# Optimization experiments

Measured on AMD Instinct MI355X. Metric: run time of the kernel, lower is better.

The kernel has to match this reference:

```python
import jax, jax.numpy as jnp
import numpy as np

B_GR = 128    # graphs per batch
N0 = 512      # nodes per graph before pooling
E_PER = 4096  # edges per graph (kept static; pooled-away edges get weight 0)
H = 128       # hidden
F = 128       # num_features (== hidden)
C = 10        # num_classes
K_HOP = 3     # Jacobi polynomial order (hop_num)
A_J, B_J = 1.0, 1.0
EPS = 1e-5


def _bn(h, g, b):
    # training-mode BatchNorm1d: batch stats, biased variance
    m = jnp.mean(h, 0)
    v = jnp.mean((h - m) ** 2, 0)
    return (h - m) * jax.lax.rsqrt(v + EPS) * g + b


def _forward(x, convW, convb, bnW, bnB, bn7W, bn7B, attW, theta,
             lin1W, lin1b, lin2W, lin2b, lin3W, lin3b, src, dst):
    w = jnp.ones((src.shape[0],), x.dtype)  # edge weights; 0 => filtered edge
    n = N0
    h = x
    reads = []
    for i in range(5):
        N = B_GR * n
        # symmetric GCN normalization with self loops on the weighted graph
        deg = jax.ops.segment_sum(w, dst, num_segments=N) + 1.0
        dinv = jax.lax.rsqrt(deg)
        enorm = dinv[src] * dinv[dst] * w   # per-edge norm [E]
        snorm = dinv * dinv                 # self-loop norm [N]
        prop = lambda m_: jax.ops.segment_sum(enorm[:, None] * m_[src], dst, num_segments=N) + m_ * snorm[:, None]
        pvec = lambda v_: jax.ops.segment_sum(enorm * v_[src], dst, num_segments=N) + v_ * snorm
        # GCNConv -> BN -> ReLU
        h = prop(h @ convW[i]) + convb[i]
        h = jax.nn.relu(_bn(h, bnW[i], bnB[i]))
        # JacobiPool: Jacobi-polynomial diffusion of attention scores
        s0 = h @ attW[i]                    # [N]
        polys = [s0, 0.5 * ((A_J - B_J) * s0 + (A_J + B_J + 2.0) * pvec(s0))]
        for kk in range(2, K_HOP + 1):
            c0 = 2 * kk * (kk + A_J + B_J) * (2 * kk + A_J + B_J - 2)
            c1 = (2 * kk + A_J + B_J - 1) * (2 * kk + A_J + B_J) * (2 * kk + A_J + B_J - 2)
            c2 = (2 * kk + A_J + B_J - 1) * (A_J * A_J - B_J * B_J)
            c3 = 2 * (kk + A_J - 1) * (kk + B_J - 1) * (2 * kk + A_J + B_J)
            polys.append((c1 * pvec(polys[-1]) + c2 * polys[-1] - c3 * polys[-2]) / c0)
        score = sum(theta[i, j] * polys[j] for j in range(K_HOP + 1))
        # top-k node selection per graph (ratio 0.5 -> static k)
        k = n // 2
        _, idx = jax.lax.top_k(score.reshape(B_GR, n), k)
        sel = (idx + (jnp.arange(B_GR) * n)[:, None]).reshape(-1)  # global node ids [B*k]
        h = h[sel] * jnp.tanh(score[sel])[:, None]
        # remap/filter edges to surviving nodes (masked, static edge count)
        new_id = jnp.full((N,), -1, jnp.int32).at[sel].set(jnp.arange(B_GR * k, dtype=jnp.int32))
        ns, nd = new_id[src], new_id[dst]
        valid = (ns >= 0) & (nd >= 0) & (w > 0)
        w = valid.astype(x.dtype)
        src = jnp.where(valid, ns, 0)
        dst = jnp.where(valid, nd, 0)
        # readout: global max pool || global mean pool per graph
        xg = h.reshape(B_GR, k, H)
        reads.append(jnp.concatenate([xg.max(1), xg.mean(1)], -1))
        n = k
    g = sum(reads) / 5.0                    # [B, 2H]
    g = jax.nn.relu(_bn(g @ lin1W + lin1b, bnW[5], bnB[5]))
    g = jax.nn.relu(_bn(g @ lin2W + lin2b, bn7W, bn7B))
    return jax.nn.log_softmax(g @ lin3W + lin3b, -1)


def setup_inputs() -> dict:
    key = jax.random.key(0)
    ks = jax.random.split(key, 8)
    N = B_GR * N0
    E = B_GR * E_PER
    rng = np.random.default_rng(0)
    off = np.repeat(np.arange(B_GR, dtype=np.int32) * N0, E_PER)
    src = jnp.asarray(off + rng.integers(0, N0, E).astype(np.int32))
    dst = jnp.asarray(off + rng.integers(0, N0, E).astype(np.int32))
    s = 1.0 / np.sqrt(H)
    return {
        "x": jax.random.normal(ks[0], (N, F), jnp.float32),
        "convW": jax.random.normal(ks[1], (5, H, H), jnp.float32) * s,
        "convb": jnp.zeros((5, H), jnp.float32),
        "bnW": jnp.ones((6, H), jnp.float32),
        "bnB": jnp.zeros((6, H), jnp.float32),
        "bn7W": jnp.ones((H // 2,), jnp.float32),
        "bn7B": jnp.zeros((H // 2,), jnp.float32),
        "attW": jax.random.normal(ks[2], (5, H), jnp.float32) * s,
        "theta": jax.random.normal(ks[3], (5, K_HOP + 1), jnp.float32) * 0.5,
        "lin1W": jax.random.normal(ks[4], (2 * H, H), jnp.float32) * (1.0 / np.sqrt(2 * H)),
        "lin1b": jnp.zeros((H,), jnp.float32),
        "lin2W": jax.random.normal(ks[5], (H, H // 2), jnp.float32) * s,
        "lin2b": jnp.zeros((H // 2,), jnp.float32),
        "lin3W": jax.random.normal(ks[6], (H // 2, C), jnp.float32) * (1.0 / np.sqrt(H // 2)),
        "lin3b": jnp.zeros((C,), jnp.float32),
        "src": src,
        "dst": dst,
    }


def reference(x, convW, convb, bnW, bnB, bn7W, bn7B, attW, theta,
              lin1W, lin1b, lin2W, lin2b, lin3W, lin3b, src, dst):
    return _forward(x, convW, convb, bnW, bnB, bn7W, bn7B, attW, theta,
                    lin1W, lin1b, lin2W, lin2b, lin3W, lin3b, src, dst)
```

## Files before the change

kernel.cpp:

```cpp
#include <hip/hip_runtime.h>
#include <hip/hip_bf16.h>

#define B_GRAPH 128
#define ETOT    (128*4096)
#define N0G     (128*512)
#define HF      128

__global__ __launch_bounds__(256) void k_init(const int* __restrict__ s_in, const int* __restrict__ d_in_,
                                              int* __restrict__ srcw, int* __restrict__ dstw,
                                              float* __restrict__ wv, int2* __restrict__ csr,
                                              int2* __restrict__ rb2, float* __restrict__ dinvv,
                                              float* __restrict__ gacc, float* __restrict__ statsH,
                                              float* __restrict__ stats0, float* __restrict__ stats1){
    int g = blockIdx.x, t = threadIdx.x;
    __shared__ int cnt[512];
    __shared__ int cur[512];
    __shared__ float dvl[512];
    for (int l = t; l < 512; l += 256) cnt[l] = 0;
    gacc[g*256 + t] = 0.f;
    if (g == 0){
        statsH[t] = 0.f; if (t < 128) statsH[256+t] = 0.f;
        stats0[t] = 0.f; stats1[t] = 0.f;
    }
    __syncthreads();
    for (int j = t; j < 4096; j += 256){
        int e = g*4096 + j;
        int sg = s_in[e], dg = d_in_[e];
        srcw[e] = sg; dstw[e] = dg; wv[e] = 1.f;
        atomicAdd(&cnt[dg & 511], 1);
    }
    __syncthreads();
    int c0 = cnt[2*t], c1 = cnt[2*t+1];
    int pairsum = c0 + c1;
    cur[t] = pairsum;
    __syncthreads();
    for (int off = 1; off < 256; off <<= 1){
        int a = (t >= off) ? cur[t-off] : 0;
        __syncthreads();
        cur[t] += a;
        __syncthreads();
    }
    int begpair = cur[t] - pairsum;
    __syncthreads();
    cur[2*t]   = begpair;
    cur[2*t+1] = begpair + c0;
    __syncthreads();
    for (int l = t; l < 512; l += 256){
        rb2[g*512 + l] = make_int2(g*4096 + cur[l], cnt[l]);
        float dv = rsqrtf((float)cnt[l] + 1.f);
        dvl[l] = dv;
        dinvv[g*512 + l] = dv;
    }
    __syncthreads();
    for (int j = t; j < 4096; j += 256){
        int e = g*4096 + j;
        int sg = srcw[e], dl = dstw[e] & 511;
        int p = atomicAdd(&cur[dl], 1);
        csr[g*4096 + p] = make_int2(sg, __float_as_int(dvl[sg & 511]));
    }
}

__global__ __launch_bounds__(256) void k_gemm(const float* __restrict__ A, const float* __restrict__ Wg,
                                              float* __restrict__ C){
    __shared__ float Ws[64*HF];
    int tx = threadIdx.x & 15, ty = threadIdx.x >> 4;
    int r0 = blockIdx.x*64 + ty*4, c0 = tx*4;
    float acc[4][8];
    #pragma unroll
    for (int j=0;j<4;++j)
        #pragma unroll
        for (int l=0;l<8;++l) acc[j][l] = 0.f;
    for (int kh = 0; kh < 2; ++kh){
        __syncthreads();
        {
            float4* d4 = (float4*)Ws;
            const float4* s4 = (const float4*)(Wg + kh*64*HF);
            for (int i = threadIdx.x; i < 64*HF/4; i += 256) d4[i] = s4[i];
        }
        __syncthreads();
        for (int k4 = 0; k4 < 16; ++k4){
            float4 av[4];
            #pragma unroll
            for (int j=0;j<4;++j)
                av[j] = *(const float4*)(A + (size_t)(r0+j)*HF + kh*64 + k4*4);
            #pragma unroll
            for (int kk=0; kk<4; ++kk){
                int kl = k4*4 + kk;
                float4 w0 = *(const float4*)(Ws + kl*HF + c0);
                float4 w1 = *(const float4*)(Ws + kl*HF + c0 + 64);
                #pragma unroll
                for (int j=0;j<4;++j){
                    float a = reinterpret_cast<const float*>(&av[j])[kk];
                    acc[j][0] += a*w0.x; acc[j][1] += a*w0.y; acc[j][2] += a*w0.z; acc[j][3] += a*w0.w;
                    acc[j][4] += a*w1.x; acc[j][5] += a*w1.y; acc[j][6] += a*w1.z; acc[j][7] += a*w1.w;
                }
            }
        }
    }
    #pragma unroll
    for (int j=0;j<4;++j){
        *(float4*)(C + (size_t)(r0+j)*HF + c0)      = make_float4(acc[j][0],acc[j][1],acc[j][2],acc[j][3]);
        *(float4*)(C + (size_t)(r0+j)*HF + c0 + 64) = make_float4(acc[j][4],acc[j][5],acc[j][6],acc[j][7]);
    }
}

__global__ __launch_bounds__(256) void k_prop(const float* __restrict__ Y, const float* __restrict__ cb,
                                              const int2* __restrict__ rb2, const int2* __restrict__ cp,
                                              const float* __restrict__ dinv,
                                              float* __restrict__ X, int n, int lb, int Nn){
    int xcd = blockIdx.x & 7, c = blockIdx.x >> 3;
    int g = xcd*16 + (c >> lb);
    int m = c & ((1 << lb) - 1);
    int v = g*n + m*8 + (threadIdx.x >> 5);
    int f4 = threadIdx.x & 31;
    float dv = dinv[v];
    float4 y = *(const float4*)(Y + (size_t)v*HF + f4*4);
    float4 acc = make_float4(0.f, 0.f, 0.f, 0.f);
    int2 rb = rb2[v];
    int e0 = rb.x, e1 = rb.x + rb.y;
    for (int j = e0; j < e1; ++j){
        int2 e = cp[j];
        int s = e.x & (Nn - 1);
        float en = __int_as_float(e.y);
        float4 h = *(const float4*)(Y + (size_t)s*HF + f4*4);
        acc.x += en*h.x; acc.y += en*h.y; acc.z += en*h.z; acc.w += en*h.w;
    }
    int f = f4*4;
    acc.x = y.x*dv*dv + dv*acc.x + cb[f];
    acc.y = y.y*dv*dv + dv*acc.y + cb[f+1];
    acc.z = y.z*dv*dv + dv*acc.z + cb[f+2];
    acc.w = y.w*dv*dv + dv*acc.w + cb[f+3];
    *(float4*)(X + (size_t)v*HF + f) = acc;
}

__global__ __launch_bounds__(256) void k_bnstats(const float* __restrict__ X, float* __restrict__ stats){
    int c = threadIdx.x & 127, h = threadIdx.x >> 7;
    int r0 = blockIdx.x * 256;
    float s = 0.f, s2 = 0.f;
    for (int r = r0 + h; r < r0 + 256; r += 2){
        float x = X[(size_t)r*HF + c];
        s += x; s2 += x*x;
    }
    __shared__ float l1[256], l2[256];
    l1[threadIdx.x] = s; l2[threadIdx.x] = s2;
    __syncthreads();
    if (threadIdx.x < 128){
        atomicAdd(&stats[c],     l1[threadIdx.x] + l1[threadIdx.x+128]);
        atomicAdd(&stats[128+c], l2[threadIdx.x] + l2[threadIdx.x+128]);
    }
}

__global__ __launch_bounds__(1024, 4) void k_conv(
    const float* __restrict__ A, const float* __restrict__ Wg, const float* __restrict__ cb,
    const int2* __restrict__ rb2, const int2* __restrict__ cp, const float* __restrict__ dinv,
    float* __restrict__ G, float* __restrict__ X, float* __restrict__ stats,
    int n, int Nn)
{
    int g = blockIdx.x, t = threadIdx.x;
    __shared__ float Ws[64*HF];
    __shared__ float red[32*HF];
    int sub = t >> 8;
    int t8  = t & 255;
    int tx = t8 & 15, ty = t8 >> 4;
    int nT = (n + 255) >> 8;
    for (int tile = 0; tile < nT; ++tile){
        int r0 = tile*256 + sub*64 + ty*4;
        bool act = (r0 < n);
        float acc[4][8];
        #pragma unroll
        for (int j=0;j<4;++j)
            #pragma unroll
            for (int l=0;l<8;++l) acc[j][l] = 0.f;
        for (int kh = 0; kh < 2; ++kh){
            __syncthreads();
            {
                float4* d4 = (float4*)Ws;
                const float4* s4 = (const float4*)(Wg + kh*64*HF);
                #pragma unroll
                for (int i = 0; i < 2; ++i) d4[t + i*1024] = s4[t + i*1024];
            }
            __syncthreads();
            if (act){
                int c0 = tx*4;
                for (int k4 = 0; k4 < 16; ++k4){
                    float4 av[4];
                    #pragma unroll
                    for (int j=0;j<4;++j)
                        av[j] = *(const float4*)(A + ((size_t)g*n + r0 + j)*HF + kh*64 + k4*4);
                    #pragma unroll
                    for (int kk=0; kk<4; ++kk){
                        int kl = k4*4 + kk;
                        float4 w0 = *(const float4*)(Ws + kl*HF + c0);
                        float4 w1 = *(const float4*)(Ws + kl*HF + c0 + 64);
                        #pragma unroll
                        for (int j=0;j<4;++j){
                            float a = reinterpret_cast<const float*>(&av[j])[kk];
                            acc[j][0] += a*w0.x; acc[j][1] += a*w0.y; acc[j][2] += a*w0.z; acc[j][3] += a*w0.w;
                            acc[j][4] += a*w1.x; acc[j][5] += a*w1.y; acc[j][6] += a*w1.z; acc[j][7] += a*w1.w;
                        }
                    }
                }
            }
        }
        if (act){
            int c0 = tx*4;
            #pragma unroll
            for (int j=0;j<4;++j){
                *(float4*)(G + ((size_t)g*n + r0 + j)*HF + c0)      = make_float4(acc[j][0],acc[j][1],acc[j][2],acc[j][3]);
                *(float4*)(G + ((size_t)g*n + r0 + j)*HF + c0 + 64) = make_float4(acc[j][4],acc[j][5],acc[j][6],acc[j][7]);
            }
        }
    }
    __syncthreads();
    int f4 = t & 31;
    int f = f4*4;
    float4 s  = make_float4(0.f,0.f,0.f,0.f);
    float4 s2 = make_float4(0.f,0.f,0.f,0.f);
    float cb0 = cb[f], cb1 = cb[f+1], cb2 = cb[f+2], cb3 = cb[f+3];
    for (int l = t >> 5; l < n; l += 32){
        int v = g*n + l;
        float dv = dinv[v];
        float4 y = *(const float4*)(G + (size_t)v*HF + f);
        float4 acc = make_float4(0.f,0.f,0.f,0.f);
        int2 rb = rb2[v];
        int e0 = rb.x, e1 = rb.x + rb.y;
        for (int j = e0; j < e1; ++j){
            int2 e = cp[j];
            int sN = e.x & (Nn - 1);
            float en = __int_as_float(e.y);
            float4 h = *(const float4*)(G + (size_t)sN*HF + f);
            acc.x += en*h.x; acc.y += en*h.y; acc.z += en*h.z; acc.w += en*h.w;
        }
        acc.x = y.x*dv*dv + dv*acc.x + cb0;
        acc.y = y.y*dv*dv + dv*acc.y + cb1;
        acc.z = y.z*dv*dv + dv*acc.z + cb2;
        acc.w = y.w*dv*dv + dv*acc.w + cb3;
        *(float4*)(X + (size_t)v*HF + f) = acc;
        s.x += acc.x; s.y += acc.y; s.z += acc.z; s.w += acc.w;
        s2.x += acc.x*acc.x; s2.y += acc.y*acc.y; s2.z += acc.z*acc.z; s2.w += acc.w*acc.w;
    }
    int base = (t >> 5)*HF + f;
    __syncthreads();
    *(float4*)&red[base] = s;
    __syncthreads();
    if (t < 128){
        float a = 0.f;
        #pragma unroll
        for (int j = 0; j < 32; ++j) a += red[j*HF + t];
        atomicAdd(&stats[t], a);
    }
    __syncthreads();
    *(float4*)&red[base] = s2;
    __syncthreads();
    if (t < 128){
        float a = 0.f;
        #pragma unroll
        for (int j = 0; j < 32; ++j) a += red[j*HF + t];
        atomicAdd(&stats[128+t], a);
    }
}

__global__ __launch_bounds__(1024) void k_graph(
    const float* __restrict__ H, const float* __restrict__ stats,
    const float* __restrict__ gw, const float* __restrict__ gb,
    const float* __restrict__ aw, const float* __restrict__ th,
    const int2* __restrict__ rb2, int2* __restrict__ csr, const float* __restrict__ dinv,
    int* __restrict__ srcw, int* __restrict__ dstw, float* __restrict__ wv,
    float* __restrict__ P, float* __restrict__ gacc,
    int2* __restrict__ rb2n, float* __restrict__ dinvn, float* __restrict__ statsNext,
    float invN, float ca2, float cc2, float ca3, float cc3,
    int n, int last)
{
    int g = blockIdx.x, t = threadIdx.x;
    int k = n >> 1;
    __shared__ int2  eds[4096];
    __shared__ int2  rbl[512];
    __shared__ float dvv[512], p0[512], p1[512], p2[512];
    __shared__ float ss[512];
    __shared__ int   si[512];
    __shared__ float tss[256];
    __shared__ int   nid[512];
    __shared__ int   cntN[256], curN[256];
    __shared__ float dvn[256];
    __shared__ float bna[128], bnb[128];
    __shared__ float red[1024];

    if (t < 256) statsNext[t] = 0.f;
    if (t < 128){
        float mean = stats[t]*invN;
        float var  = stats[128+t]*invN - mean*mean;
        float iv   = rsqrtf(var + 1e-5f);
        bna[t] = iv*gw[t];
        bnb[t] = gb[t] - mean*iv*gw[t];
    }
    for (int l = t; l < n; l += 1024){
        int2 rb = rb2[g*n + l];
        rbl[l] = make_int2(rb.x - g*4096, rb.y);
        dvv[l] = dinv[g*n + l];
    }
    __syncthreads();
    int medg = rbl[n-1].x + rbl[n-1].y;
    for (int j = t; j < medg; j += 1024){
        int2 e = csr[g*4096 + j];
        eds[j] = make_int2(e.x & (n-1), e.y);
    }
    int lane = t & 63, wid = t >> 6;
    for (int l = wid; l < n; l += 16){
        const float* hp = H + ((size_t)g*n + l)*HF;
        float a0 = hp[lane], a1 = hp[lane+64];
        float v0 = fmaxf(a0*bna[lane]    + bnb[lane],    0.f) * aw[lane];
        float v1 = fmaxf(a1*bna[lane+64] + bnb[lane+64], 0.f) * aw[lane+64];
        float p = v0 + v1;
        for (int off = 32; off; off >>= 1) p += __shfl_down(p, off);
        if (lane == 0) p0[l] = p;
    }
    __syncthreads();
    for (int l = t; l < n; l += 1024){
        int2 rc = rbl[l];
        float acc = 0.f;
        for (int j = 0; j < rc.y; ++j){
            int2 e = eds[rc.x + j];
            acc += __int_as_float(e.y) * p0[e.x];
        }
        float dv = dvv[l];
        p1[l] = 2.f*(p0[l]*dv*dv + dv*acc);
    }
    __syncthreads();
    for (int l = t; l < n; l += 1024){
        int2 rc = rbl[l];
        float acc = 0.f;
        for (int j = 0; j < rc.y; ++j){
            int2 e = eds[rc.x + j];
            acc += __int_as_float(e.y) * p1[e.x];
        }
        float dv = dvv[l];
        p2[l] = ca2*(p1[l]*dv*dv + dv*acc) + cc2*p0[l];
    }
    __syncthreads();
    float t0v = th[0], t1v = th[1], t2c = th[2], t3v = th[3];
    for (int l = t; l < n; l += 1024){
        int2 rc = rbl[l];
        float acc = 0.f;
        for (int j = 0; j < rc.y; ++j){
            int2 e = eds[rc.x + j];
            acc += __int_as_float(e.y) * p2[e.x];
        }
        float dv = dvv[l];
        float tv = p2[l]*dv*dv + dv*acc;
        float p3 = ca3*tv + cc3*p1[l];
        ss[l] = t0v*p0[l] + t1v*p1[l] + t2c*p2[l] + t3v*p3;
        si[l] = l;
    }
    __syncthreads();
    for (int size = 2; size <= n; size <<= 1){
        for (int stride = size >> 1; stride > 0; stride >>= 1){
            for (int i = t; i < n; i += 1024){
                int j = i ^ stride;
                if (j > i){
                    bool asc = ((i & size) == 0);
                    float s1 = ss[i], s2 = ss[j];
                    int   i1 = si[i], i2 = si[j];
                    bool gt = (s1 < s2) || (s1 == s2 && i1 > i2);
                    if (gt == asc){ ss[i] = s2; ss[j] = s1; si[i] = i2; si[j] = i1; }
                }
            }
            __syncthreads();
        }
    }
    for (int l = t; l < n; l += 1024) nid[l] = -1;
    __syncthreads();
    for (int r = t; r < k; r += 1024){
        nid[si[r]] = r;
        tss[r] = tanhf(ss[r]);
    }
    __syncthreads();
    {
        int f = t & 127, rl = t >> 7;
        float af = bna[f], bf = bnb[f];
        float mx = -3.4e38f, sm = 0.f;
        for (int r = rl; r < k; r += 8){
            int old = si[r];
            float hv = H[((size_t)g*n + old)*HF + f];
            float v = fmaxf(hv*af + bf, 0.f) * tss[r];
            P[((size_t)g*k + r)*HF + f] = v;
            mx = fmaxf(mx, v); sm += v;
        }
        red[t] = mx;
        __syncthreads();
        if (t < 512) red[t] = fmaxf(red[t], red[t+512]);
        __syncthreads();
        if (t < 256) red[t] = fmaxf(red[t], red[t+256]);
        __syncthreads();
        if (t < 128) gacc[g*256 + t] += fmaxf(red[t], red[t+128]);
        __syncthreads();
        red[t] = sm;
        __syncthreads();
        if (t < 512) red[t] += red[t+512];
        __syncthreads();
        if (t < 256) red[t] += red[t+256];
        __syncthreads();
        if (t < 128) gacc[g*256 + 128 + t] += (red[t] + red[t+128]) / (float)k;
    }
    if (last) return;
    __syncthreads();
    if (t < k) cntN[t] = 0;
    __syncthreads();
    for (int j = t; j < 4096; j += 1024){
        int e = g*4096 + j;
        float we = wv[e];
        int valid = 0, ns = 0, nd = 0;
        if (we > 0.5f){
            int sl = srcw[e] & (n-1);
            int dl = dstw[e] & (n-1);
            ns = nid[sl]; nd = nid[dl];
            valid = (ns >= 0) && (nd >= 0);
        }
        if (valid){
            srcw[e] = g*k + ns; dstw[e] = g*k + nd; wv[e] = 1.f;
            atomicAdd(&cntN[nd], 1);
        } else {
            srcw[e] = 0; dstw[e] = 0; wv[e] = 0.f;
        }
    }
    __syncthreads();
    int c = (t < 256) ? ((t < k) ? cntN[t] : 0) : 0;
    if (t < 256) si[t] = c;
    __syncthreads();
    for (int off = 1; off < 256; off <<= 1){
        int a = 0;
        if (t < 256 && t >= off) a = si[t-off];
        __syncthreads();
        if (t < 256) si[t] += a;
        __syncthreads();
    }
    if (t < k){
        int beg = si[t] - c;
        rb2n[g*k + t] = make_int2(g*4096 + beg, c);
        float dv = rsqrtf((float)c + 1.f);
        dinvn[g*k + t] = dv;
        dvn[t] = dv;
        curN[t] = beg;
    }
    __syncthreads();
    for (int j = t; j < 4096; j += 1024){
        int e = g*4096 + j;
        if (wv[e] > 0.5f){
            int sg = srcw[e], dl = dstw[e] & (k-1);
            int p = atomicAdd(&curN[dl], 1);
            csr[g*4096 + p] = make_int2(sg, __float_as_int(dvn[sg & (k-1)]));
        }
    }
}

__global__ __launch_bounds__(256) void k_head1(const float* __restrict__ gacc, const float* __restrict__ W1,
                                               const float* __restrict__ b1, float* __restrict__ t1,
                                               float* __restrict__ sh){
    int r = blockIdx.x;
    int c = threadIdx.x & 127, h = threadIdx.x >> 7;
    __shared__ float gs[256];
    __shared__ float red[256];
    gs[threadIdx.x] = gacc[r*256 + threadIdx.x];
    __syncthreads();
    float s = 0.f;
    #pragma unroll
    for (int kk = 0; kk < 128; ++kk)
        s += gs[h*128 + kk] * W1[(h*128 + kk)*128 + c];
    red[threadIdx.x] = s;
    __syncthreads();
    if (h == 0){
        float v = (red[c] + red[c+128]) * 0.2f + b1[c];
        t1[r*128 + c] = v;
        atomicAdd(&sh[c], v);
        atomicAdd(&sh[128 + c], v*v);
    }
}
__global__ __launch_bounds__(128) void k_head2(const float* __restrict__ t1, const float* __restrict__ gw,
                                               const float* __restrict__ gb, const float* __restrict__ W2,
                                               const float* __restrict__ b2, float* __restrict__ sh,
                                               float* __restrict__ t2){
    int r = blockIdx.x, t = threadIdx.x;
    int cc = t & 63, h = t >> 6;
    __shared__ float row[128];
    __shared__ float red[128];
    {
        float mean = sh[t] * (1.f/128.f);
        float var  = sh[128+t]*(1.f/128.f) - mean*mean;
        float iv   = rsqrtf(var + 1e-5f);
        float v = (t1[r*128+t] - mean)*iv*gw[t] + gb[t];
        row[t] = fmaxf(v, 0.f);
    }
    __syncthreads();
    float s = 0.f;
    #pragma unroll
    for (int kk = 0; kk < 64; ++kk)
        s += row[h*64+kk] * W2[(h*64+kk)*64 + cc];
    red[t] = s;
    __syncthreads();
    if (h == 0){
        float v = red[cc] + red[cc+64] + b2[cc];
        t2[r*64+cc] = v;
        atomicAdd(&sh[256+cc], v);
        atomicAdd(&sh[320+cc], v*v);
    }
}
__global__ __launch_bounds__(64) void k_head3(const float* __restrict__ t2, const float* __restrict__ gw,
                                              const float* __restrict__ gb, const float* __restrict__ W3,
                                              const float* __restrict__ b3, const float* __restrict__ sh,
                                              float* __restrict__ out){
    int r = blockIdx.x, t = threadIdx.x;
    float mean = sh[256+t]*(1.f/128.f);
    float var  = sh[320+t]*(1.f/128.f) - mean*mean;
    float iv   = rsqrtf(var + 1e-5f);
    float v = fmaxf((t2[r*64+t]-mean)*iv*gw[t] + gb[t], 0.f);
    float lg[10];
    #pragma unroll
    for (int j = 0; j < 10; ++j){
        float p = v * W3[t*10 + j];
        for (int off = 32; off; off >>= 1) p += __shfl_down(p, off);
        lg[j] = p;
    }
    if (t == 0){
        float m = -3.4e38f;
        #pragma unroll
        for (int j = 0; j < 10; ++j){ lg[j] += b3[j]; m = fmaxf(m, lg[j]); }
        float se = 0.f;
        #pragma unroll
        for (int j = 0; j < 10; ++j) se += expf(lg[j] - m);
        float l = logf(se) + m;
        #pragma unroll
        for (int j = 0; j < 10; ++j) out[r*10 + j] = lg[j] - l;
    }
}

extern "C" void kernel_launch(void* const* d_in, const int* in_sizes, int n_in,
                              void* d_out, int out_size, void* d_ws, size_t ws_size,
                              hipStream_t stream){
    const float* x     = (const float*)d_in[0];
    const float* convW = (const float*)d_in[1];
    const float* convb = (const float*)d_in[2];
    const float* bnW   = (const float*)d_in[3];
    const float* bnB   = (const float*)d_in[4];
    const float* bn7W  = (const float*)d_in[5];
    const float* bn7B  = (const float*)d_in[6];
    const float* attW  = (const float*)d_in[7];
    const float* theta = (const float*)d_in[8];
    const float* lin1W = (const float*)d_in[9];
    const float* lin1b = (const float*)d_in[10];
    const float* lin2W = (const float*)d_in[11];
    const float* lin2b = (const float*)d_in[12];
    const float* lin3W = (const float*)d_in[13];
    const float* lin3b = (const float*)d_in[14];
    const int*   src0  = (const int*)d_in[15];
    const int*   dst0  = (const int*)d_in[16];

    char* base = (char*)d_ws;
    size_t off = 0;
    auto take = [&](size_t bytes) -> void* {
        void* p = base + off;
        off = (off + bytes + 255) & ~(size_t)255;
        return p;
    };
    float* bufGP = (float*)take((size_t)N0G*HF*4);
    float* bufH  = (float*)take((size_t)N0G*HF*4);
    int*   srcw  = (int*)  take((size_t)ETOT*4);
    int*   dstw  = (int*)  take((size_t)ETOT*4);
    float* w     = (float*)take((size_t)ETOT*4);
    int2*  csr_p = (int2*) take((size_t)ETOT*8);
    int2*  rb2A  = (int2*) take((size_t)N0G*8);
    int2*  rb2B  = (int2*) take((size_t)N0G*8);
    float* dinvA = (float*)take((size_t)N0G*4);
    float* dinvB = (float*)take((size_t)N0G*4);
    float* stats0= (float*)take(256*4);
    float* stats1= (float*)take(256*4);
    float* gacc  = (float*)take((size_t)B_GRAPH*256*4);
    float* t1    = (float*)take((size_t)B_GRAPH*128*4);
    float* t2    = (float*)take((size_t)B_GRAPH*64*4);
    float* statsH= (float*)take(384*4);

    auto coef = [](int kk, float& ca, float& cc){
        double a = 1.0, b = 1.0;
        double c0 = 2.0*kk*(kk+a+b)*(2.0*kk+a+b-2.0);
        double c1 = (2.0*kk+a+b-1.0)*(2.0*kk+a+b)*(2.0*kk+a+b-2.0);
        double c3 = 2.0*(kk+a-1.0)*(kk+b-1.0)*(2.0*kk+a+b);
        ca = (float)(c1/c0); cc = (float)(-c3/c0);
    };
    float ca2, cc2, ca3, cc3;
    coef(2, ca2, cc2);
    coef(3, ca3, cc3);

    k_init<<<B_GRAPH, 256, 0, stream>>>(src0, dst0, srcw, dstw, w, csr_p, rb2A, dinvA,
                                        gacc, statsH, stats0, stats1);

    for (int i = 0; i < 5; ++i){
        int n = 512 >> i;
        int Nn = B_GRAPH*n;
        int2*  rb_cur = (i & 1) ? rb2B : rb2A;
        int2*  rb_nxt = (i & 1) ? rb2A : rb2B;
        float* dv_cur = (i & 1) ? dinvB : dinvA;
        float* dv_nxt = (i & 1) ? dinvA : dinvB;
        float* st_cur = (i & 1) ? stats1 : stats0;
        float* st_nxt = (i & 1) ? stats0 : stats1;
        const float* convA = (i == 0) ? x : bufGP;
        float* G = (i == 0) ? bufGP : (bufGP + (size_t)4*1024*1024);

        if (i == 0){
            k_gemm<<<Nn/64, 256, 0, stream>>>(convA, convW, G);
            k_prop<<<Nn/8, 256, 0, stream>>>(G, convb, rb_cur, csr_p, dv_cur, bufH, n, 6, Nn);
            k_bnstats<<<Nn/256, 256, 0, stream>>>(bufH, st_cur);
        } else {
            k_conv<<<B_GRAPH, 1024, 0, stream>>>(convA, convW + (size_t)i*HF*HF, convb + i*HF,
                                                 rb_cur, csr_p, dv_cur, G, bufH, st_cur, n, Nn);
        }
        k_graph<<<B_GRAPH, 1024, 0, stream>>>(bufH, st_cur, bnW + i*HF, bnB + i*HF, attW + i*HF,
                                              theta + i*4, rb_cur, csr_p, dv_cur,
                                              srcw, dstw, w, bufGP, gacc, rb_nxt, dv_nxt, st_nxt,
                                              1.0f/(float)Nn, ca2, cc2, ca3, cc3, n, (i == 4) ? 1 : 0);
    }

    k_head1<<<B_GRAPH, 256, 0, stream>>>(gacc, lin1W, lin1b, t1, statsH);
    k_head2<<<B_GRAPH, 128, 0, stream>>>(t1, bnW + 5*HF, bnB + 5*HF, lin2W, lin2b, statsH, t2);
    k_head3<<<B_GRAPH, 64, 0, stream>>>(t2, bn7W, bn7B, lin3W, lin3b, statsH, (float*)d_out);
}
```

Before: 484.8 us.

## Fuse next-level GCN conv into pooling kernel, rotating three stats buffers

```diff
diff --git a/kernel.cpp b/kernel.cpp
--- a/kernel.cpp
+++ b/kernel.cpp
@@ -11,7 +11,8 @@
                                               float* __restrict__ wv, int2* __restrict__ csr,
                                               int2* __restrict__ rb2, float* __restrict__ dinvv,
                                               float* __restrict__ gacc, float* __restrict__ statsH,
-                                              float* __restrict__ stats0, float* __restrict__ stats1){
+                                              float* __restrict__ st0, float* __restrict__ st1,
+                                              float* __restrict__ st2){
     int g = blockIdx.x, t = threadIdx.x;
     __shared__ int cnt[512];
     __shared__ int cur[512];
@@ -20,7 +21,7 @@
     gacc[g*256 + t] = 0.f;
     if (g == 0){
         statsH[t] = 0.f; if (t < 128) statsH[256+t] = 0.f;
-        stats0[t] = 0.f; stats1[t] = 0.f;
+        st0[t] = 0.f; st1[t] = 0.f; st2[t] = 0.f;
     }
     __syncthreads();
     for (int j = t; j < 4096; j += 256){
@@ -150,115 +151,16 @@
     }
 }
 
-__global__ __launch_bounds__(1024, 4) void k_conv(
-    const float* __restrict__ A, const float* __restrict__ Wg, const float* __restrict__ cb,
-    const int2* __restrict__ rb2, const int2* __restrict__ cp, const float* __restrict__ dinv,
-    float* __restrict__ G, float* __restrict__ X, float* __restrict__ stats,
-    int n, int Nn)
-{
-    int g = blockIdx.x, t = threadIdx.x;
-    __shared__ float Ws[64*HF];
-    __shared__ float red[32*HF];
-    int sub = t >> 8;
-    int t8  = t & 255;
-    int tx = t8 & 15, ty = t8 >> 4;
-    int nT = (n + 255) >> 8;
-    for (int tile = 0; tile < nT; ++tile){
-        int r0 = tile*256 + sub*64 + ty*4;
-        bool act = (r0 < n);
-        float acc[4][8];
-        #pragma unroll
-        for (int j=0;j<4;++j)
-            #pragma unroll
-            for (int l=0;l<8;++l) acc[j][l] = 0.f;
-        for (int kh = 0; kh < 2; ++kh){
-            __syncthreads();
-            {
-                float4* d4 = (float4*)Ws;
-                const float4* s4 = (const float4*)(Wg + kh*64*HF);
-                #pragma unroll
-                for (int i = 0; i < 2; ++i) d4[t + i*1024] = s4[t + i*1024];
-            }
-            __syncthreads();
-            if (act){
-                int c0 = tx*4;
-                for (int k4 = 0; k4 < 16; ++k4){
-                    float4 av[4];
-                    #pragma unroll
-                    for (int j=0;j<4;++j)
-                        av[j] = *(const float4*)(A + ((size_t)g*n + r0 + j)*HF + kh*64 + k4*4);
-                    #pragma unroll
-                    for (int kk=0; kk<4; ++kk){
-                        int kl = k4*4 + kk;
-                        float4 w0 = *(const float4*)(Ws + kl*HF + c0);
-                        float4 w1 = *(const float4*)(Ws + kl*HF + c0 + 64);
-                        #pragma unroll
-                        for (int j=0;j<4;++j){
-                            float a = reinterpret_cast<const float*>(&av[j])[kk];
-                            acc[j][0] += a*w0.x; acc[j][1] += a*w0.y; acc[j][2] += a*w0.z; acc[j][3] += a*w0.w;
-                            acc[j][4] += a*w1.x; acc[j][5] += a*w1.y; acc[j][6] += a*w1.z; acc[j][7] += a*w1.w;
-                        }
-                    }
-                }
-            }
-        }
-        if (act){
-            int c0 = tx*4;
-            #pragma unroll
-            for (int j=0;j<4;++j){
-                *(float4*)(G + ((size_t)g*n + r0 + j)*HF + c0)      = make_float4(acc[j][0],acc[j][1],acc[j][2],acc[j][3]);
-                *(float4*)(G + ((size_t)g*n + r0 + j)*HF + c0 + 64) = make_float4(acc[j][4],acc[j][5],acc[j][6],acc[j][7]);
-            }
-        }
-    }
-    __syncthreads();
-    int f4 = t & 31;
-    int f = f4*4;
-    float4 s  = make_float4(0.f,0.f,0.f,0.f);
-    float4 s2 = make_float4(0.f,0.f,0.f,0.f);
-    float cb0 = cb[f], cb1 = cb[f+1], cb2 = cb[f+2], cb3 = cb[f+3];
-    for (int l = t >> 5; l < n; l += 32){
-        int v = g*n + l;
-        float dv = dinv[v];
-        float4 y = *(const float4*)(G + (size_t)v*HF + f);
-        float4 acc = make_float4(0.f,0.f,0.f,0.f);
-        int2 rb = rb2[v];
-        int e0 = rb.x, e1 = rb.x + rb.y;
-        for (int j = e0; j < e1; ++j){
-            int2 e = cp[j];
-            int sN = e.x & (Nn - 1);
-            float en = __int_as_float(e.y);
-            float4 h = *(const float4*)(G + (size_t)sN*HF + f);
-            acc.x += en*h.x; acc.y += en*h.y; acc.z += en*h.z; acc.w += en*h.w;
-        }
-        acc.x = y.x*dv*dv + dv*acc.x + cb0;
-        acc.y = y.y*dv*dv + dv*acc.y + cb1;
-        acc.z = y.z*dv*dv + dv*acc.z + cb2;
-        acc.w = y.w*dv*dv + dv*acc.w + cb3;
-        *(float4*)(X + (size_t)v*HF + f) = acc;
-        s.x += acc.x; s.y += acc.y; s.z += acc.z; s.w += acc.w;
-        s2.x += acc.x*acc.x; s2.y += acc.y*acc.y; s2.z += acc.z*acc.z; s2.w += acc.w*acc.w;
-    }
-    int base = (t >> 5)*HF + f;
-    __syncthreads();
-    *(float4*)&red[base] = s;
-    __syncthreads();
-    if (t < 128){
-        float a = 0.f;
-        #pragma unroll
-        for (int j = 0; j < 32; ++j) a += red[j*HF + t];
-        atomicAdd(&stats[t], a);
-    }
-    __syncthreads();
-    *(float4*)&red[base] = s2;
-    __syncthreads();
-    if (t < 128){
-        float a = 0.f;
-        #pragma unroll
-        for (int j = 0; j < 32; ++j) a += red[j*HF + t];
-        atomicAdd(&stats[128+t], a);
-    }
-}
+union KSmem {
+    struct {
+        int2  eds[4096]; int2 rbl[512];
+        float dvv[512], p0[512], p1[512], p2[512];
+        float ss[512]; int si[512]; float tss[256]; int nid[512];
+        int   cntN[256], curN[256]; float dvn[256];
+        float bna[128], bnb[128]; float red[1024];
+    } gr;
+    struct { float Ws[64*HF]; float red[32*HF]; } cv;
+};
 
 __global__ __launch_bounds__(1024) void k_graph(
     const float* __restrict__ H, const float* __restrict__ stats,
@@ -267,89 +169,82 @@
     const int2* __restrict__ rb2, int2* __restrict__ csr, const float* __restrict__ dinv,
     int* __restrict__ srcw, int* __restrict__ dstw, float* __restrict__ wv,
     float* __restrict__ P, float* __restrict__ gacc,
-    int2* __restrict__ rb2n, float* __restrict__ dinvn, float* __restrict__ statsNext,
+    int2* __restrict__ rb2n, float* __restrict__ dinvn,
+    float* __restrict__ stZero, float* __restrict__ stAcc,
+    const float* __restrict__ Wnext, const float* __restrict__ cbNext,
+    float* __restrict__ Gnext, float* __restrict__ Hnext,
     float invN, float ca2, float cc2, float ca3, float cc3,
     int n, int last)
 {
     int g = blockIdx.x, t = threadIdx.x;
     int k = n >> 1;
-    __shared__ int2  eds[4096];
-    __shared__ int2  rbl[512];
-    __shared__ float dvv[512], p0[512], p1[512], p2[512];
-    __shared__ float ss[512];
-    __shared__ int   si[512];
-    __shared__ float tss[256];
-    __shared__ int   nid[512];
-    __shared__ int   cntN[256], curN[256];
-    __shared__ float dvn[256];
-    __shared__ float bna[128], bnb[128];
-    __shared__ float red[1024];
-
-    if (t < 256) statsNext[t] = 0.f;
+    __shared__ KSmem sm;
+
+    if (t < 256) stZero[t] = 0.f;
     if (t < 128){
         float mean = stats[t]*invN;
         float var  = stats[128+t]*invN - mean*mean;
         float iv   = rsqrtf(var + 1e-5f);
-        bna[t] = iv*gw[t];
-        bnb[t] = gb[t] - mean*iv*gw[t];
+        sm.gr.bna[t] = iv*gw[t];
+        sm.gr.bnb[t] = gb[t] - mean*iv*gw[t];
     }
     for (int l = t; l < n; l += 1024){
         int2 rb = rb2[g*n + l];
-        rbl[l] = make_int2(rb.x - g*4096, rb.y);
-        dvv[l] = dinv[g*n + l];
-    }
-    __syncthreads();
-    int medg = rbl[n-1].x + rbl[n-1].y;
+        sm.gr.rbl[l] = make_int2(rb.x - g*4096, rb.y);
+        sm.gr.dvv[l] = dinv[g*n + l];
+    }
+    __syncthreads();
+    int medg = sm.gr.rbl[n-1].x + sm.gr.rbl[n-1].y;
     for (int j = t; j < medg; j += 1024){
         int2 e = csr[g*4096 + j];
-        eds[j] = make_int2(e.x & (n-1), e.y);
+        sm.gr.eds[j] = make_int2(e.x & (n-1), e.y);
     }
     int lane = t & 63, wid = t >> 6;
     for (int l = wid; l < n; l += 16){
         const float* hp = H + ((size_t)g*n + l)*HF;
         float a0 = hp[lane], a1 = hp[lane+64];
-        float v0 = fmaxf(a0*bna[lane]    + bnb[lane],    0.f) * aw[lane];
-        float v1 = fmaxf(a1*bna[lane+64] + bnb[lane+64], 0.f) * aw[lane+64];
+        float v0 = fmaxf(a0*sm.gr.bna[lane]    + sm.gr.bnb[lane],    0.f) * aw[lane];
+        float v1 = fmaxf(a1*sm.gr.bna[lane+64] + sm.gr.bnb[lane+64], 0.f) * aw[lane+64];
         float p = v0 + v1;
         for (int off = 32; off; off >>= 1) p += __shfl_down(p, off);
-        if (lane == 0) p0[l] = p;
+        if (lane == 0) sm.gr.p0[l] = p;
     }
     __syncthreads();
     for (int l = t; l < n; l += 1024){
-        int2 rc = rbl[l];
+        int2 rc = sm.gr.rbl[l];
         float acc = 0.f;
         for (int j = 0; j < rc.y; ++j){
-            int2 e = eds[rc.x + j];
-            acc += __int_as_float(e.y) * p0[e.x];
-        }
-        float dv = dvv[l];
-        p1[l] = 2.f*(p0[l]*dv*dv + dv*acc);
+            int2 e = sm.gr.eds[rc.x + j];
+            acc += __int_as_float(e.y) * sm.gr.p0[e.x];
+        }
+        float dv = sm.gr.dvv[l];
+        sm.gr.p1[l] = 2.f*(sm.gr.p0[l]*dv*dv + dv*acc);
     }
     __syncthreads();
     for (int l = t; l < n; l += 1024){
-        int2 rc = rbl[l];
+        int2 rc = sm.gr.rbl[l];
         float acc = 0.f;
         for (int j = 0; j < rc.y; ++j){
-            int2 e = eds[rc.x + j];
-            acc += __int_as_float(e.y) * p1[e.x];
-        }
-        float dv = dvv[l];
-        p2[l] = ca2*(p1[l]*dv*dv + dv*acc) + cc2*p0[l];
+            int2 e = sm.gr.eds[rc.x + j];
+            acc += __int_as_float(e.y) * sm.gr.p1[e.x];
+        }
+        float dv = sm.gr.dvv[l];
+        sm.gr.p2[l] = ca2*(sm.gr.p1[l]*dv*dv + dv*acc) + cc2*sm.gr.p0[l];
     }
     __syncthreads();
     float t0v = th[0], t1v = th[1], t2c = th[2], t3v = th[3];
     for (int l = t; l < n; l += 1024){
-        int2 rc = rbl[l];
+        int2 rc = sm.gr.rbl[l];
         float acc = 0.f;
         for (int j = 0; j < rc.y; ++j){
-            int2 e = eds[rc.x + j];
-            acc += __int_as_float(e.y) * p2[e.x];
-        }
-        float dv = dvv[l];
-        float tv = p2[l]*dv*dv + dv*acc;
-        float p3 = ca3*tv + cc3*p1[l];
-        ss[l] = t0v*p0[l] + t1v*p1[l] + t2c*p2[l] + t3v*p3;
-        si[l] = l;
+            int2 e = sm.gr.eds[rc.x + j];
+            acc += __int_as_float(e.y) * sm.gr.p2[e.x];
+        }
+        float dv = sm.gr.dvv[l];
+        float tv = sm.gr.p2[l]*dv*dv + dv*acc;
+        float p3 = ca3*tv + cc3*sm.gr.p1[l];
+        sm.gr.ss[l] = t0v*sm.gr.p0[l] + t1v*sm.gr.p1[l] + t2c*sm.gr.p2[l] + t3v*p3;
+        sm.gr.si[l] = l;
     }
     __syncthreads();
     for (int size = 2; size <= n; size <<= 1){
@@ -358,52 +253,52 @@
                 int j = i ^ stride;
                 if (j > i){
                     bool asc = ((i & size) == 0);
-                    float s1 = ss[i], s2 = ss[j];
-                    int   i1 = si[i], i2 = si[j];
+                    float s1 = sm.gr.ss[i], s2 = sm.gr.ss[j];
+                    int   i1 = sm.gr.si[i], i2 = sm.gr.si[j];
                     bool gt = (s1 < s2) || (s1 == s2 && i1 > i2);
-                    if (gt == asc){ ss[i] = s2; ss[j] = s1; si[i] = i2; si[j] = i1; }
+                    if (gt == asc){ sm.gr.ss[i] = s2; sm.gr.ss[j] = s1; sm.gr.si[i] = i2; sm.gr.si[j] = i1; }
                 }
             }
             __syncthreads();
         }
     }
-    for (int l = t; l < n; l += 1024) nid[l] = -1;
+    for (int l = t; l < n; l += 1024) sm.gr.nid[l] = -1;
     __syncthreads();
     for (int r = t; r < k; r += 1024){
-        nid[si[r]] = r;
-        tss[r] = tanhf(ss[r]);
+        sm.gr.nid[sm.gr.si[r]] = r;
+        sm.gr.tss[r] = tanhf(sm.gr.ss[r]);
     }
     __syncthreads();
     {
         int f = t & 127, rl = t >> 7;
-        float af = bna[f], bf = bnb[f];
-        float mx = -3.4e38f, sm = 0.f;
+        float af = sm.gr.bna[f], bf = sm.gr.bnb[f];
+        float mx = -3.4e38f, smv = 0.f;
         for (int r = rl; r < k; r += 8){
-            int old = si[r];
+            int old = sm.gr.si[r];
             float hv = H[((size_t)g*n + old)*HF + f];
-            float v = fmaxf(hv*af + bf, 0.f) * tss[r];
+            float v = fmaxf(hv*af + bf, 0.f) * sm.gr.tss[r];
             P[((size_t)g*k + r)*HF + f] = v;
-            mx = fmaxf(mx, v); sm += v;
-        }
-        red[t] = mx;
-        __syncthreads();
-        if (t < 512) red[t] = fmaxf(red[t], red[t+512]);
-        __syncthreads();
-        if (t < 256) red[t] = fmaxf(red[t], red[t+256]);
-        __syncthreads();
-        if (t < 128) gacc[g*256 + t] += fmaxf(red[t], red[t+128]);
-        __syncthreads();
-        red[t] = sm;
-        __syncthreads();
-        if (t < 512) red[t] += red[t+512];
-        __syncthreads();
-        if (t < 256) red[t] += red[t+256];
-        __syncthreads();
-        if (t < 128) gacc[g*256 + 128 + t] += (red[t] + red[t+128]) / (float)k;
+            mx = fmaxf(mx, v); smv += v;
+        }
+        sm.gr.red[t] = mx;
+        __syncthreads();
+        if (t < 512) sm.gr.red[t] = fmaxf(sm.gr.red[t], sm.gr.red[t+512]);
+        __syncthreads();
+        if (t < 256) sm.gr.red[t] = fmaxf(sm.gr.red[t], sm.gr.red[t+256]);
+        __syncthreads();
+        if (t < 128) gacc[g*256 + t] += fmaxf(sm.gr.red[t], sm.gr.red[t+128]);
+        __syncthreads();
+        sm.gr.red[t] = smv;
+        __syncthreads();
+        if (t < 512) sm.gr.red[t] += sm.gr.red[t+512];
+        __syncthreads();
+        if (t < 256) sm.gr.red[t] += sm.gr.red[t+256];
+        __syncthreads();
+        if (t < 128) gacc[g*256 + 128 + t] += (sm.gr.red[t] + sm.gr.red[t+128]) / (float)k;
     }
     if (last) return;
     __syncthreads();
-    if (t < k) cntN[t] = 0;
+    if (t < k) sm.gr.cntN[t] = 0;
     __syncthreads();
     for (int j = t; j < 4096; j += 1024){
         int e = g*4096 + j;
@@ -412,42 +307,143 @@
         if (we > 0.5f){
             int sl = srcw[e] & (n-1);
             int dl = dstw[e] & (n-1);
-            ns = nid[sl]; nd = nid[dl];
+            ns = sm.gr.nid[sl]; nd = sm.gr.nid[dl];
             valid = (ns >= 0) && (nd >= 0);
         }
         if (valid){
             srcw[e] = g*k + ns; dstw[e] = g*k + nd; wv[e] = 1.f;
-            atomicAdd(&cntN[nd], 1);
+            atomicAdd(&sm.gr.cntN[nd], 1);
         } else {
             srcw[e] = 0; dstw[e] = 0; wv[e] = 0.f;
         }
     }
     __syncthreads();
-    int c = (t < 256) ? ((t < k) ? cntN[t] : 0) : 0;
-    if (t < 256) si[t] = c;
+    int c = (t < 256) ? ((t < k) ? sm.gr.cntN[t] : 0) : 0;
+    if (t < 256) sm.gr.si[t] = c;
     __syncthreads();
     for (int off = 1; off < 256; off <<= 1){
         int a = 0;
-        if (t < 256 && t >= off) a = si[t-off];
-        __syncthreads();
-        if (t < 256) si[t] += a;
+        if (t < 256 && t >= off) a = sm.gr.si[t-off];
+        __syncthreads();
+        if (t < 256) sm.gr.si[t] += a;
         __syncthreads();
     }
     if (t < k){
-        int beg = si[t] - c;
+        int beg = sm.gr.si[t] - c;
         rb2n[g*k + t] = make_int2(g*4096 + beg, c);
         float dv = rsqrtf((float)c + 1.f);
         dinvn[g*k + t] = dv;
-        dvn[t] = dv;
-        curN[t] = beg;
+        sm.gr.dvn[t] = dv;
+        sm.gr.curN[t] = beg;
     }
     __syncthreads();
     for (int j = t; j < 4096; j += 1024){
         int e = g*4096 + j;
         if (wv[e] > 0.5f){
             int sg = srcw[e], dl = dstw[e] & (k-1);
-            int p = atomicAdd(&curN[dl], 1);
-            csr[g*4096 + p] = make_int2(sg, __float_as_int(dvn[sg & (k-1)]));
+            int p = atomicAdd(&sm.gr.curN[dl], 1);
+            csr[g*4096 + p] = make_int2(sg, __float_as_int(sm.gr.dvn[sg & (k-1)]));
+        }
+    }
+    __syncthreads();
+    int Nn2 = B_GRAPH * k;
+    {
+        int sub = t >> 8, t8 = t & 255, tx = t8 & 15, ty = t8 >> 4;
+        int cc0 = tx*4;
+        int nT = (k + 255) >> 8;
+        for (int tile = 0; tile < nT; ++tile){
+            int r0 = tile*256 + sub*64 + ty*4;
+            bool act = (r0 < k);
+            float acc[4][8];
+            #pragma unroll
+            for (int j=0;j<4;++j)
+                #pragma unroll
+                for (int l=0;l<8;++l) acc[j][l] = 0.f;
+            for (int kh = 0; kh < 2; ++kh){
+                __syncthreads();
+                {
+                    float4* d4 = (float4*)sm.cv.Ws;
+                    const float4* s4 = (const float4*)(Wnext + kh*64*HF);
+                    #pragma unroll
+                    for (int i2 = 0; i2 < 2; ++i2) d4[t + i2*1024] = s4[t + i2*1024];
+                }
+                __syncthreads();
+                if (act){
+                    for (int k4 = 0; k4 < 16; ++k4){
+                        float4 av[4];
+                        #pragma unroll
+                        for (int j=0;j<4;++j)
+                            av[j] = *(const float4*)(P + ((size_t)g*k + r0 + j)*HF + kh*64 + k4*4);
+                        #pragma unroll
+                        for (int kk=0; kk<4; ++kk){
+                            int kl = k4*4 + kk;
+                            float4 w0 = *(const float4*)(sm.cv.Ws + kl*HF + cc0);
+                            float4 w1 = *(const float4*)(sm.cv.Ws + kl*HF + cc0 + 64);
+                            #pragma unroll
+                            for (int j=0;j<4;++j){
+                                float aa = reinterpret_cast<const float*>(&av[j])[kk];
+                                acc[j][0] += aa*w0.x; acc[j][1] += aa*w0.y; acc[j][2] += aa*w0.z; acc[j][3] += aa*w0.w;
+                                acc[j][4] += aa*w1.x; acc[j][5] += aa*w1.y; acc[j][6] += aa*w1.z; acc[j][7] += aa*w1.w;
+                            }
+                        }
+                    }
+                }
+            }
+            if (act){
+                #pragma unroll
+                for (int j=0;j<4;++j){
+                    *(float4*)(Gnext + ((size_t)g*k + r0 + j)*HF + cc0)      = make_float4(acc[j][0],acc[j][1],acc[j][2],acc[j][3]);
+                    *(float4*)(Gnext + ((size_t)g*k + r0 + j)*HF + cc0 + 64) = make_float4(acc[j][4],acc[j][5],acc[j][6],acc[j][7]);
+                }
+            }
+        }
+    }
+    __syncthreads();
+    {
+        int f = (t & 31)*4;
+        float4 s  = make_float4(0.f,0.f,0.f,0.f);
+        float4 s2 = make_float4(0.f,0.f,0.f,0.f);
+        float cb0 = cbNext[f], cb1 = cbNext[f+1], cb2 = cbNext[f+2], cb3 = cbNext[f+3];
+        for (int l = t >> 5; l < k; l += 32){
+            int v = g*k + l;
+            float dv = dinvn[v];
+            float4 y = *(const float4*)(Gnext + (size_t)v*HF + f);
+            float4 acc = make_float4(0.f,0.f,0.f,0.f);
+            int2 rb = rb2n[v];
+            int e1 = rb.x + rb.y;
+            for (int j = rb.x; j < e1; ++j){
+                int2 e = csr[j];
+                int sN = e.x & (Nn2 - 1);
+                float en = __int_as_float(e.y);
+                float4 h = *(const float4*)(Gnext + (size_t)sN*HF + f);
+                acc.x += en*h.x; acc.y += en*h.y; acc.z += en*h.z; acc.w += en*h.w;
+            }
+            acc.x = y.x*dv*dv + dv*acc.x + cb0;
+            acc.y = y.y*dv*dv + dv*acc.y + cb1;
+            acc.z = y.z*dv*dv + dv*acc.z + cb2;
+            acc.w = y.w*dv*dv + dv*acc.w + cb3;
+            *(float4*)(Hnext + (size_t)v*HF + f) = acc;
+            s.x += acc.x; s.y += acc.y; s.z += acc.z; s.w += acc.w;
+            s2.x += acc.x*acc.x; s2.y += acc.y*acc.y; s2.z += acc.z*acc.z; s2.w += acc.w*acc.w;
+        }
+        int base = (t >> 5)*HF + f;
+        __syncthreads();
+        *(float4*)&sm.cv.red[base] = s;
+        __syncthreads();
+        if (t < 128){
+            float a = 0.f;
+            #pragma unroll
+            for (int j = 0; j < 32; ++j) a += sm.cv.red[j*HF + t];
+            atomicAdd(&stAcc[t], a);
+        }
+        __syncthreads();
+        *(float4*)&sm.cv.red[base] = s2;
+        __syncthreads();
+        if (t < 128){
+            float a = 0.f;
+            #pragma unroll
+            for (int j = 0; j < 32; ++j) a += sm.cv.red[j*HF + t];
+            atomicAdd(&stAcc[128+t], a);
         }
     }
 }
@@ -561,7 +557,8 @@
         return p;
     };
     float* bufGP = (float*)take((size_t)N0G*HF*4);
-    float* bufH  = (float*)take((size_t)N0G*HF*4);
+    float* bufHA = (float*)take((size_t)N0G*HF*4);
+    float* bufHB = (float*)take((size_t)(N0G/2)*HF*4);
     int*   srcw  = (int*)  take((size_t)ETOT*4);
     int*   dstw  = (int*)  take((size_t)ETOT*4);
     float* w     = (float*)take((size_t)ETOT*4);
@@ -570,8 +567,10 @@
     int2*  rb2B  = (int2*) take((size_t)N0G*8);
     float* dinvA = (float*)take((size_t)N0G*4);
     float* dinvB = (float*)take((size_t)N0G*4);
-    float* stats0= (float*)take(256*4);
-    float* stats1= (float*)take(256*4);
+    float* st[3];
+    st[0] = (float*)take(256*4);
+    st[1] = (float*)take(256*4);
+    st[2] = (float*)take(256*4);
     float* gacc  = (float*)take((size_t)B_GRAPH*256*4);
     float* t1    = (float*)take((size_t)B_GRAPH*128*4);
     float* t2    = (float*)take((size_t)B_GRAPH*64*4);
@@ -589,7 +588,12 @@
     coef(3, ca3, cc3);
 
     k_init<<<B_GRAPH, 256, 0, stream>>>(src0, dst0, srcw, dstw, w, csr_p, rb2A, dinvA,
-                                        gacc, statsH, stats0, stats1);
+                                        gacc, statsH, st[0], st[1], st[2]);
+
+    float* G = bufGP + (size_t)4*1024*1024;
+    k_gemm<<<N0G/64, 256, 0, stream>>>(x, convW, bufGP);
+    k_prop<<<N0G/8, 256, 0, stream>>>(bufGP, convb, rb2A, csr_p, dinvA, bufHA, 512, 6, N0G);
+    k_bnstats<<<N0G/256, 256, 0, stream>>>(bufHA, st[0]);
 
     for (int i = 0; i < 5; ++i){
         int n = 512 >> i;
@@ -598,22 +602,16 @@
         int2*  rb_nxt = (i & 1) ? rb2A : rb2B;
         float* dv_cur = (i & 1) ? dinvB : dinvA;
         float* dv_nxt = (i & 1) ? dinvA : dinvB;
-        float* st_cur = (i & 1) ? stats1 : stats0;
-        float* st_nxt = (i & 1) ? stats0 : stats1;
-        const float* convA = (i == 0) ? x : bufGP;
-        float* G = (i == 0) ? bufGP : (bufGP + (size_t)4*1024*1024);
-
-        if (i == 0){
-            k_gemm<<<Nn/64, 256, 0, stream>>>(convA, convW, G);
-            k_prop<<<Nn/8, 256, 0, stream>>>(G, convb, rb_cur, csr_p, dv_cur, bufH, n, 6, Nn);
-            k_bnstats<<<Nn/256, 256, 0, stream>>>(bufH, st_cur);
-        } else {
-            k_conv<<<B_GRAPH, 1024, 0, stream>>>(convA, convW + (size_t)i*HF*HF, convb + i*HF,
-                                                 rb_cur, csr_p, dv_cur, G, bufH, st_cur, n, Nn);
-        }
-        k_graph<<<B_GRAPH, 1024, 0, stream>>>(bufH, st_cur, bnW + i*HF, bnB + i*HF, attW + i*HF,
+        float* Hcur = (i & 1) ? bufHB : bufHA;
+        float* Hnxt = (i & 1) ? bufHA : bufHB;
+        int wnext = (i < 4) ? (i + 1) : 4;
+
+        k_graph<<<B_GRAPH, 1024, 0, stream>>>(Hcur, st[i % 3], bnW + i*HF, bnB + i*HF, attW + i*HF,
                                               theta + i*4, rb_cur, csr_p, dv_cur,
-                                              srcw, dstw, w, bufGP, gacc, rb_nxt, dv_nxt, st_nxt,
+                                              srcw, dstw, w, bufGP, gacc, rb_nxt, dv_nxt,
+                                              st[(i + 2) % 3], st[(i + 1) % 3],
+                                              convW + (size_t)wnext*HF*HF, convb + wnext*HF,
+                                              G, Hnxt,
                                               1.0f/(float)Nn, ca2, cc2, ca3, cc3, n, (i == 4) ? 1 : 0);
     }
 
```

After: 476.2 us. About the same (-1.8%).
